# Kernel tuning notes

Hardware: AMD Instinct MI355X
Metric: run time of the kernel (lower is better)

The kernel has to match this reference:

```python
import jax, jax.numpy as jnp
import numpy as np

B, D, H = 512, 512, 512  # batch, input dim, hidden dim


def setup_inputs() -> dict:
    key = jax.random.key(0)
    ks = jax.random.split(key, 7)
    s = 1.0 / np.sqrt(D)
    return {
        "x": jax.random.normal(ks[0], (B, D), jnp.float32),
        "W1": jax.random.normal(ks[1], (D, H), jnp.float32) * s,
        "b1": jax.random.normal(ks[2], (H,), jnp.float32) * 0.01,
        "W2": jax.random.normal(ks[3], (H, H), jnp.float32) * s,
        "b2": jax.random.normal(ks[4], (H,), jnp.float32) * 0.01,
        "w3": jax.random.normal(ks[5], (H,), jnp.float32) * s,
        "b3": jax.random.normal(ks[6], (1,), jnp.float32) * 0.01,
    }


def _per_sample(xi, W1, b1, W2, b2, w3, b3):
    # Sequential layers applied to one sample; per-sample scalar loss.
    h = jax.nn.relu(xi @ W1 + b1)
    h = jax.nn.relu(h @ W2 + b2)
    return h @ w3 + b3[0]


def reference(x, W1, b1, W2, b2, w3, b3):
    # Forward pass (vectorized over the batch) -> per-sample losses [B].
    h = jax.nn.relu(x @ W1 + b1)
    h = jax.nn.relu(h @ W2 + b2)
    output = h @ w3 + b3[0]  # [B]

    # _autogram: per-sample Jacobian w.r.t. all layer parameters with a seed
    # of ones (grad = ones_like(output)); gramian accumulates J @ J.T per
    # parameter block. jax.vmap(jax.grad) == torch.vmap(vjp) with scalar seed 1.
    grad_fn = jax.grad(_per_sample, argnums=(1, 2, 3, 4, 5, 6))
    grads = jax.vmap(grad_fn, in_axes=(0, None, None, None, None, None, None))(
        x, W1, b1, W2, b2, w3, b3
    )  # pytree of per-sample grads, each leaf [B, *param_shape]

    bsz = x.shape[0]
    gramian = jnp.zeros((bsz, bsz), x.dtype)
    for g in grads:  # fixed small number of parameter tensors (matches per-layer loop)
        J = g.reshape(bsz, -1)  # [B, n_params_block]
        gramian = gramian + J @ J.T
    return output, gramian
```

## Files before the change

kernel.cpp:

```cpp
#include <hip/hip_runtime.h>


#define NN 512

typedef __attribute__((ext_vector_type(8))) short v8s;
typedef __attribute__((ext_vector_type(4))) float v4f;

static __device__ __forceinline__ unsigned short f2bf(float f) {
    union { float f; unsigned u; } v; v.f = f;
    unsigned r = v.u + 0x7FFF + ((v.u >> 16) & 1);
    return (unsigned short)(r >> 16);
}
static __device__ __forceinline__ float bf2f(unsigned short h) {
    union { unsigned u; float f; } v; v.u = ((unsigned)h) << 16;
    return v.f;
}

#define MFMA(a, b, c) __builtin_amdgcn_mfma_f32_16x16x32_bf16(a, b, c, 0, 0, 0)

__global__ __launch_bounds__(256) void prep(
    const float* __restrict__ x, const float* __restrict__ W1,
    const float* __restrict__ W2, const float* __restrict__ b3,
    unsigned short* __restrict__ xhi, unsigned short* __restrict__ xlo,
    unsigned short* __restrict__ W1th, unsigned short* __restrict__ W1tl,
    unsigned short* __restrict__ W2th, unsigned short* __restrict__ W2tl,
    unsigned short* __restrict__ W2b, float* __restrict__ out) {
    __shared__ float T[32][33];
    const int t = threadIdx.x;
    const int lr = t >> 3, lc = (t & 7) * 4;
    const int r0 = blockIdx.y * 32, c0 = blockIdx.x * 32;
    const int z = blockIdx.z;
    if (z == 2) {
        float4 v = *(const float4*)&x[(r0 + lr) * NN + c0 + lc];
        ushort4 hi, lo;
        hi.x = f2bf(v.x); lo.x = f2bf(v.x - bf2f(hi.x));
        hi.y = f2bf(v.y); lo.y = f2bf(v.y - bf2f(hi.y));
        hi.z = f2bf(v.z); lo.z = f2bf(v.z - bf2f(hi.z));
        hi.w = f2bf(v.w); lo.w = f2bf(v.w - bf2f(hi.w));
        *(ushort4*)&xhi[(r0 + lr) * NN + c0 + lc] = hi;
        *(ushort4*)&xlo[(r0 + lr) * NN + c0 + lc] = lo;
        if (blockIdx.x == 0 && t < 32) out[r0 + t] = b3[0];
        return;
    }
    const float* src = (z == 1) ? W2 : W1;
    float4 v = *(const float4*)&src[(r0 + lr) * NN + c0 + lc];
    if (z == 1) {
        ushort4 h;
        h.x = f2bf(v.x); h.y = f2bf(v.y); h.z = f2bf(v.z); h.w = f2bf(v.w);
        *(ushort4*)&W2b[(r0 + lr) * NN + c0 + lc] = h;
    }
    T[lr][lc + 0] = v.x; T[lr][lc + 1] = v.y;
    T[lr][lc + 2] = v.z; T[lr][lc + 3] = v.w;
    __syncthreads();
    unsigned short* dh = (z == 1) ? W2th : W1th;
    unsigned short* dl = (z == 1) ? W2tl : W1tl;
    float a0 = T[lc + 0][lr], a1 = T[lc + 1][lr];
    float a2 = T[lc + 2][lr], a3 = T[lc + 3][lr];
    ushort4 hi, lo;
    hi.x = f2bf(a0); lo.x = f2bf(a0 - bf2f(hi.x));
    hi.y = f2bf(a1); lo.y = f2bf(a1 - bf2f(hi.y));
    hi.z = f2bf(a2); lo.z = f2bf(a2 - bf2f(hi.z));
    hi.w = f2bf(a3); lo.w = f2bf(a3 - bf2f(hi.w));
    *(ushort4*)&dh[(c0 + lr) * NN + r0 + lc] = hi;
    *(ushort4*)&dl[(c0 + lr) * NN + r0 + lc] = lo;
}

__global__ __launch_bounds__(1024, 4) void fwd1x(
    const unsigned short* __restrict__ Ahi, const unsigned short* __restrict__ Alo,
    const unsigned short* __restrict__ Bhi, const unsigned short* __restrict__ Blo,
    const float* __restrict__ bias,
    unsigned short* __restrict__ Chi, unsigned short* __restrict__ Clo,
    float* __restrict__ SXX) {
    __shared__ float red[12][64][4];
    const int t = threadIdx.x;
    const int wave = t >> 6, lane = t & 63;
    const int q = wave & 3, s = wave >> 2;
    const int r = lane & 15, quad = lane >> 4;
    const int i0 = blockIdx.y * 32 + 16 * (q >> 1);
    const int j0 = blockIdx.x * 32 + 16 * (q & 1);
    const int ao = (i0 + r) * NN + quad * 8 + s * 128;
    const int bo = (j0 + r) * NN + quad * 8 + s * 128;
    if (blockIdx.z == 1) {
        v4f acc = {0.f, 0.f, 0.f, 0.f};
        #pragma unroll
        for (int k0 = 0; k0 < 128; k0 += 32) {
            v8s a = *(const v8s*)(Ahi + ao + k0);
            v8s b = *(const v8s*)(Ahi + bo + k0);
            acc = MFMA(a, b, acc);
        }
        if (s > 0) *(v4f*)red[(s - 1) * 4 + q][lane] = acc;
        __syncthreads();
        if (s == 0) {
            v4f a0 = acc + *(v4f*)red[q][lane] + *(v4f*)red[4 + q][lane]
                         + *(v4f*)red[8 + q][lane];
            #pragma unroll
            for (int rr = 0; rr < 4; ++rr)
                SXX[(i0 + quad * 4 + rr) * NN + j0 + r] = a0[rr];
        }
        return;
    }
    v4f hh = {0.f, 0.f, 0.f, 0.f}, lh = hh, hl = hh;
    #pragma unroll
    for (int k0 = 0; k0 < 128; k0 += 32) {
        v8s ah = *(const v8s*)(Ahi + ao + k0);
        v8s al = *(const v8s*)(Alo + ao + k0);
        v8s bh = *(const v8s*)(Bhi + bo + k0);
        v8s bl = *(const v8s*)(Blo + bo + k0);
        hh = MFMA(ah, bh, hh);
        lh = MFMA(al, bh, lh);
        hl = MFMA(ah, bl, hl);
    }
    v4f z;
    #pragma unroll
    for (int rr = 0; rr < 4; ++rr) z[rr] = (hh[rr] + lh[rr]) + hl[rr];
    if (s > 0) *(v4f*)red[(s - 1) * 4 + q][lane] = z;
    __syncthreads();
    if (s == 0) {
        v4f z0 = z + *(v4f*)red[q][lane] + *(v4f*)red[4 + q][lane]
                   + *(v4f*)red[8 + q][lane];
        const float bj = bias[j0 + r];
        #pragma unroll
        for (int rr = 0; rr < 4; ++rr) {
            const int i = i0 + quad * 4 + rr, j = j0 + r;
            float zv = z0[rr] + bj;
            float h = zv > 0.f ? zv : 0.f;
            unsigned short hi = f2bf(h);
            Chi[i * NN + j] = hi;
            Clo[i * NN + j] = f2bf(h - bf2f(hi));
        }
    }
}

__global__ __launch_bounds__(1024, 4) void fwd2(
    const unsigned short* __restrict__ Ahi, const unsigned short* __restrict__ Alo,
    const unsigned short* __restrict__ Bhi, const unsigned short* __restrict__ Blo,
    const float* __restrict__ b2, const float* __restrict__ w3,
    unsigned short* __restrict__ H2b, unsigned short* __restrict__ G2b,
    float* __restrict__ out) {
    __shared__ float red[12][64][4];
    const int t = threadIdx.x;
    const int wave = t >> 6, lane = t & 63;
    const int q = wave & 3, s = wave >> 2;
    const int r = lane & 15, quad = lane >> 4;
    const int i0 = blockIdx.y * 32 + 16 * (q >> 1);
    const int j0 = blockIdx.x * 32 + 16 * (q & 1);
    const int ao = (i0 + r) * NN + quad * 8 + s * 128;
    const int bo = (j0 + r) * NN + quad * 8 + s * 128;
    v4f hh = {0.f, 0.f, 0.f, 0.f}, lh = hh, hl = hh;
    #pragma unroll
    for (int k0 = 0; k0 < 128; k0 += 32) {
        v8s ah = *(const v8s*)(Ahi + ao + k0);
        v8s al = *(const v8s*)(Alo + ao + k0);
        v8s bh = *(const v8s*)(Bhi + bo + k0);
        v8s bl = *(const v8s*)(Blo + bo + k0);
        hh = MFMA(ah, bh, hh);
        lh = MFMA(al, bh, lh);
        hl = MFMA(ah, bl, hl);
    }
    v4f z;
    #pragma unroll
    for (int rr = 0; rr < 4; ++rr) z[rr] = (hh[rr] + lh[rr]) + hl[rr];
    if (s > 0) *(v4f*)red[(s - 1) * 4 + q][lane] = z;
    __syncthreads();
    if (s == 0) {
        v4f z0 = z + *(v4f*)red[q][lane] + *(v4f*)red[4 + q][lane]
                   + *(v4f*)red[8 + q][lane];
        const float bj = b2[j0 + r];
        const float wj = w3[j0 + r];
        const unsigned short wjb = f2bf(wj);
        #pragma unroll
        for (int rr = 0; rr < 4; ++rr) {
            const int i = i0 + quad * 4 + rr, j = j0 + r;
            float zv = z0[rr] + bj;
            float h = zv > 0.f ? zv : 0.f;
            H2b[i * NN + j] = f2bf(h);
            G2b[i * NN + j] = (zv > 0.f) ? wjb : (unsigned short)0;
            float p = h * wj;
            p += __shfl_xor(p, 1, 64);
            p += __shfl_xor(p, 2, 64);
            p += __shfl_xor(p, 4, 64);
            p += __shfl_xor(p, 8, 64);
            if (r == 0) atomicAdd(&out[i], p);
        }
    }
}

__global__ __launch_bounds__(1024, 4) void g1p(
    const unsigned short* __restrict__ G2b, const unsigned short* __restrict__ W2b,
    const unsigned short* __restrict__ H1b, const unsigned short* __restrict__ H2b,
    unsigned short* __restrict__ G1b, float* __restrict__ P) {
    __shared__ float red[12][64][3][4];
    const int t = threadIdx.x;
    const int wave = t >> 6, lane = t & 63;
    const int q = wave & 3, s = wave >> 2;
    const int r = lane & 15, quad = lane >> 4;
    const int i0 = blockIdx.y * 32 + 16 * (q >> 1);
    const int j0 = blockIdx.x * 32 + 16 * (q & 1);
    const int ao = (i0 + r) * NN + quad * 8 + s * 128;
    const int bo = (j0 + r) * NN + quad * 8 + s * 128;
    if (blockIdx.z == 1) {
        v4f a1 = {0.f, 0.f, 0.f, 0.f}, a3 = a1, a4 = a1;
        #pragma unroll
        for (int k0 = 0; k0 < 128; k0 += 32) {
            v8s ha = *(const v8s*)(H1b + ao + k0), hb = *(const v8s*)(H1b + bo + k0);
            v8s ua = *(const v8s*)(H2b + ao + k0), ub = *(const v8s*)(H2b + bo + k0);
            v8s va = *(const v8s*)(G2b + ao + k0), vb = *(const v8s*)(G2b + bo + k0);
            a1 = MFMA(ha, hb, a1);
            a3 = MFMA(ua, ub, a3);
            a4 = MFMA(va, vb, a4);
        }
        if (s > 0) {
            const int idx = (s - 1) * 4 + q;
            *(v4f*)red[idx][lane][0] = a1;
            *(v4f*)red[idx][lane][1] = a3;
            *(v4f*)red[idx][lane][2] = a4;
        }
        __syncthreads();
        if (s == 0) {
            #pragma unroll
            for (int u = 0; u < 3; ++u) {
                const int idx = u * 4 + q;
                a1 += *(v4f*)red[idx][lane][0];
                a3 += *(v4f*)red[idx][lane][1];
                a4 += *(v4f*)red[idx][lane][2];
            }
            #pragma unroll
            for (int rr = 0; rr < 4; ++rr) {
                const int i = i0 + quad * 4 + rr, j = j0 + r;
                P[i * NN + j] = a3[rr] + a4[rr] * (1.f + a1[rr]);
            }
        }
        return;
    }
    v4f acc = {0.f, 0.f, 0.f, 0.f};
    #pragma unroll
    for (int k0 = 0; k0 < 128; k0 += 32) {
        v8s a = *(const v8s*)(G2b + ao + k0);
        v8s b = *(const v8s*)(W2b + bo + k0);
        acc = MFMA(a, b, acc);
    }
    if (s > 0) *(v4f*)red[(s - 1) * 4 + q][lane][0] = acc;
    __syncthreads();
    if (s == 0) {
        v4f a0 = acc + *(v4f*)red[q][lane][0] + *(v4f*)red[4 + q][lane][0]
                     + *(v4f*)red[8 + q][lane][0];
        #pragma unroll
        for (int rr = 0; rr < 4; ++rr) {
            const int i = i0 + quad * 4 + rr;
            const int c = j0 + r;
            float v = (H1b[i * NN + c] != 0) ? a0[rr] : 0.f;
            G1b[i * NN + c] = f2bf(v);
        }
    }
}

__global__ __launch_bounds__(1024, 4) void gramf(
    const unsigned short* __restrict__ G1b, const float* __restrict__ SXX,
    const float* __restrict__ P, float* __restrict__ gram) {
    __shared__ float red[12][64][4];
    const int t = threadIdx.x;
    const int wave = t >> 6, lane = t & 63;
    const int q = wave & 3, s = wave >> 2;
    const int r = lane & 15, quad = lane >> 4;
    const int i0 = blockIdx.y * 32 + 16 * (q >> 1);
    const int j0 = blockIdx.x * 32 + 16 * (q & 1);
    const int ao = (i0 + r) * NN + quad * 8 + s * 128;
    const int bo = (j0 + r) * NN + quad * 8 + s * 128;
    v4f acc = {0.f, 0.f, 0.f, 0.f};
    #pragma unroll
    for (int k0 = 0; k0 < 128; k0 += 32) {
        v8s a = *(const v8s*)(G1b + ao + k0);
        v8s b = *(const v8s*)(G1b + bo + k0);
        acc = MFMA(a, b, acc);
    }
    if (s > 0) *(v4f*)red[(s - 1) * 4 + q][lane] = acc;
    __syncthreads();
    if (s == 0) {
        v4f a2 = acc + *(v4f*)red[q][lane] + *(v4f*)red[4 + q][lane]
                     + *(v4f*)red[8 + q][lane];
        #pragma unroll
        for (int rr = 0; rr < 4; ++rr) {
            const int i = i0 + quad * 4 + rr, j = j0 + r;
            gram[i * NN + j] = 1.f + P[i * NN + j] + a2[rr] * (1.f + SXX[i * NN + j]);
        }
    }
}

extern "C" void kernel_launch(void* const* d_in, const int* in_sizes, int n_in,
                              void* d_out, int out_size, void* d_ws, size_t ws_size,
                              hipStream_t stream) {
    const float* x  = (const float*)d_in[0];
    const float* W1 = (const float*)d_in[1];
    const float* b1 = (const float*)d_in[2];
    const float* W2 = (const float*)d_in[3];
    const float* b2 = (const float*)d_in[4];
    const float* w3 = (const float*)d_in[5];
    const float* b3 = (const float*)d_in[6];

    float* out  = (float*)d_out;
    float* gram = out + NN;

    unsigned short* p    = (unsigned short*)d_ws;
    unsigned short* xhi  = p;  p += NN * NN;
    unsigned short* xlo  = p;  p += NN * NN;
    unsigned short* W1th = p;  p += NN * NN;
    unsigned short* W1tl = p;  p += NN * NN;
    unsigned short* W2th = p;  p += NN * NN;
    unsigned short* W2tl = p;  p += NN * NN;
    unsigned short* W2b  = p;  p += NN * NN;
    unsigned short* H1b  = p;  p += NN * NN;
    unsigned short* H1lo = p;  p += NN * NN;
    unsigned short* H2b  = p;  p += NN * NN;
    unsigned short* G2b  = p;  p += NN * NN;
    unsigned short* G1b  = p;  p += NN * NN;
    float* SXX = (float*)p;  p += 2 * NN * NN;
    float* Pf  = (float*)p;  p += 2 * NN * NN;

    prep <<<dim3(16, 16, 3), dim3(256), 0, stream>>>(
        x, W1, W2, b3, xhi, xlo, W1th, W1tl, W2th, W2tl, W2b, out);
    fwd1x<<<dim3(16, 16, 2), dim3(1024), 0, stream>>>(
        xhi, xlo, W1th, W1tl, b1, H1b, H1lo, SXX);
    fwd2 <<<dim3(16, 16), dim3(1024), 0, stream>>>(
        H1b, H1lo, W2th, W2tl, b2, w3, H2b, G2b, out);
    g1p  <<<dim3(16, 16, 2), dim3(1024), 0, stream>>>(
        G2b, W2b, H1b, H2b, G1b, Pf);
    gramf<<<dim3(16, 16), dim3(1024), 0, stream>>>(
        G1b, SXX, Pf, gram);
}
```

Before: 115.8 us.

## Compute x·xᵀ Gram in prep kernel and convert x to bf16 on the fly in fwd1

Removes the xhi/xlo bf16 workspace copies of x. The x·xᵀ product (SXX) is now computed inside the prep kernel by 4-wave blocks running a full-K MFMA loop that converts fp32 x to bf16 in registers. fwd1 now loads fp32 x directly and splits it into hi/lo bf16 in registers, and drops its z=1 SXX half. This saves global writes and reads of the converted x and halves the fwd1 grid. In exchange, prep's z=2 blocks do a long serial K=512 loop with only 4 waves, and fwd1 reads twice the bytes for x and repeats the conversion.

```diff
diff --git a/kernel.cpp b/kernel.cpp
--- a/kernel.cpp
+++ b/kernel.cpp
@@ -18,30 +18,61 @@
 
 #define MFMA(a, b, c) __builtin_amdgcn_mfma_f32_16x16x32_bf16(a, b, c, 0, 0, 0)
 
+static __device__ __forceinline__ v8s load8_hi(const float* p) {
+    float4 a = *(const float4*)p;
+    float4 b = *(const float4*)(p + 4);
+    v8s h;
+    h[0] = (short)f2bf(a.x); h[1] = (short)f2bf(a.y);
+    h[2] = (short)f2bf(a.z); h[3] = (short)f2bf(a.w);
+    h[4] = (short)f2bf(b.x); h[5] = (short)f2bf(b.y);
+    h[6] = (short)f2bf(b.z); h[7] = (short)f2bf(b.w);
+    return h;
+}
+static __device__ __forceinline__ void load8_split(const float* p, v8s& h, v8s& l) {
+    float4 a = *(const float4*)p;
+    float4 b = *(const float4*)(p + 4);
+    unsigned short h0 = f2bf(a.x), h1 = f2bf(a.y), h2 = f2bf(a.z), h3 = f2bf(a.w);
+    unsigned short h4 = f2bf(b.x), h5 = f2bf(b.y), h6 = f2bf(b.z), h7 = f2bf(b.w);
+    h[0] = (short)h0; h[1] = (short)h1; h[2] = (short)h2; h[3] = (short)h3;
+    h[4] = (short)h4; h[5] = (short)h5; h[6] = (short)h6; h[7] = (short)h7;
+    l[0] = (short)f2bf(a.x - bf2f(h0)); l[1] = (short)f2bf(a.y - bf2f(h1));
+    l[2] = (short)f2bf(a.z - bf2f(h2)); l[3] = (short)f2bf(a.w - bf2f(h3));
+    l[4] = (short)f2bf(b.x - bf2f(h4)); l[5] = (short)f2bf(b.y - bf2f(h5));
+    l[6] = (short)f2bf(b.z - bf2f(h6)); l[7] = (short)f2bf(b.w - bf2f(h7));
+}
+
 __global__ __launch_bounds__(256) void prep(
     const float* __restrict__ x, const float* __restrict__ W1,
     const float* __restrict__ W2, const float* __restrict__ b3,
-    unsigned short* __restrict__ xhi, unsigned short* __restrict__ xlo,
     unsigned short* __restrict__ W1th, unsigned short* __restrict__ W1tl,
     unsigned short* __restrict__ W2th, unsigned short* __restrict__ W2tl,
-    unsigned short* __restrict__ W2b, float* __restrict__ out) {
+    unsigned short* __restrict__ W2b, float* __restrict__ SXX,
+    float* __restrict__ out) {
     __shared__ float T[32][33];
     const int t = threadIdx.x;
-    const int lr = t >> 3, lc = (t & 7) * 4;
     const int r0 = blockIdx.y * 32, c0 = blockIdx.x * 32;
     const int z = blockIdx.z;
     if (z == 2) {
-        float4 v = *(const float4*)&x[(r0 + lr) * NN + c0 + lc];
-        ushort4 hi, lo;
-        hi.x = f2bf(v.x); lo.x = f2bf(v.x - bf2f(hi.x));
-        hi.y = f2bf(v.y); lo.y = f2bf(v.y - bf2f(hi.y));
-        hi.z = f2bf(v.z); lo.z = f2bf(v.z - bf2f(hi.z));
-        hi.w = f2bf(v.w); lo.w = f2bf(v.w - bf2f(hi.w));
-        *(ushort4*)&xhi[(r0 + lr) * NN + c0 + lc] = hi;
-        *(ushort4*)&xlo[(r0 + lr) * NN + c0 + lc] = lo;
+        const int wave = t >> 6, lane = t & 63;
+        const int r = lane & 15, quad = lane >> 4;
+        const int i0 = r0 + 16 * (wave >> 1);
+        const int j0 = c0 + 16 * (wave & 1);
+        const float* ar = x + (i0 + r) * NN + quad * 8;
+        const float* br = x + (j0 + r) * NN + quad * 8;
+        v4f acc = {0.f, 0.f, 0.f, 0.f};
+        #pragma unroll
+        for (int k0 = 0; k0 < NN; k0 += 32) {
+            v8s a = load8_hi(ar + k0);
+            v8s b = load8_hi(br + k0);
+            acc = MFMA(a, b, acc);
+        }
+        #pragma unroll
+        for (int rr = 0; rr < 4; ++rr)
+            SXX[(i0 + quad * 4 + rr) * NN + j0 + r] = acc[rr];
         if (blockIdx.x == 0 && t < 32) out[r0 + t] = b3[0];
         return;
     }
+    const int lr = t >> 3, lc = (t & 7) * 4;
     const float* src = (z == 1) ? W2 : W1;
     float4 v = *(const float4*)&src[(r0 + lr) * NN + c0 + lc];
     if (z == 1) {
@@ -65,12 +96,11 @@
     *(ushort4*)&dl[(c0 + lr) * NN + r0 + lc] = lo;
 }
 
-__global__ __launch_bounds__(1024, 4) void fwd1x(
-    const unsigned short* __restrict__ Ahi, const unsigned short* __restrict__ Alo,
+__global__ __launch_bounds__(1024, 4) void fwd1(
+    const float* __restrict__ x,
     const unsigned short* __restrict__ Bhi, const unsigned short* __restrict__ Blo,
     const float* __restrict__ bias,
-    unsigned short* __restrict__ Chi, unsigned short* __restrict__ Clo,
-    float* __restrict__ SXX) {
+    unsigned short* __restrict__ Chi, unsigned short* __restrict__ Clo) {
     __shared__ float red[12][64][4];
     const int t = threadIdx.x;
     const int wave = t >> 6, lane = t & 63;
@@ -78,32 +108,13 @@
     const int r = lane & 15, quad = lane >> 4;
     const int i0 = blockIdx.y * 32 + 16 * (q >> 1);
     const int j0 = blockIdx.x * 32 + 16 * (q & 1);
-    const int ao = (i0 + r) * NN + quad * 8 + s * 128;
+    const float* ar = x + (i0 + r) * NN + quad * 8 + s * 128;
     const int bo = (j0 + r) * NN + quad * 8 + s * 128;
-    if (blockIdx.z == 1) {
-        v4f acc = {0.f, 0.f, 0.f, 0.f};
-        #pragma unroll
-        for (int k0 = 0; k0 < 128; k0 += 32) {
-            v8s a = *(const v8s*)(Ahi + ao + k0);
-            v8s b = *(const v8s*)(Ahi + bo + k0);
-            acc = MFMA(a, b, acc);
-        }
-        if (s > 0) *(v4f*)red[(s - 1) * 4 + q][lane] = acc;
-        __syncthreads();
-        if (s == 0) {
-            v4f a0 = acc + *(v4f*)red[q][lane] + *(v4f*)red[4 + q][lane]
-                         + *(v4f*)red[8 + q][lane];
-            #pragma unroll
-            for (int rr = 0; rr < 4; ++rr)
-                SXX[(i0 + quad * 4 + rr) * NN + j0 + r] = a0[rr];
-        }
-        return;
-    }
     v4f hh = {0.f, 0.f, 0.f, 0.f}, lh = hh, hl = hh;
     #pragma unroll
     for (int k0 = 0; k0 < 128; k0 += 32) {
-        v8s ah = *(const v8s*)(Ahi + ao + k0);
-        v8s al = *(const v8s*)(Alo + ao + k0);
+        v8s ah, al;
+        load8_split(ar + k0, ah, al);
         v8s bh = *(const v8s*)(Bhi + bo + k0);
         v8s bl = *(const v8s*)(Blo + bo + k0);
         hh = MFMA(ah, bh, hh);
@@ -301,8 +312,6 @@
     float* gram = out + NN;
 
     unsigned short* p    = (unsigned short*)d_ws;
-    unsigned short* xhi  = p;  p += NN * NN;
-    unsigned short* xlo  = p;  p += NN * NN;
     unsigned short* W1th = p;  p += NN * NN;
     unsigned short* W1tl = p;  p += NN * NN;
     unsigned short* W2th = p;  p += NN * NN;
@@ -317,9 +326,9 @@
     float* Pf  = (float*)p;  p += 2 * NN * NN;
 
     prep <<<dim3(16, 16, 3), dim3(256), 0, stream>>>(
-        x, W1, W2, b3, xhi, xlo, W1th, W1tl, W2th, W2tl, W2b, out);
-    fwd1x<<<dim3(16, 16, 2), dim3(1024), 0, stream>>>(
-        xhi, xlo, W1th, W1tl, b1, H1b, H1lo, SXX);
+        x, W1, W2, b3, W1th, W1tl, W2th, W2tl, W2b, SXX, out);
+    fwd1 <<<dim3(16, 16), dim3(1024), 0, stream>>>(
+        x, W1th, W1tl, b1, H1b, H1lo);
     fwd2 <<<dim3(16, 16), dim3(1024), 0, stream>>>(
         H1b, H1lo, W2th, W2tl, b2, w3, H2b, G2b, out);
     g1p  <<<dim3(16, 16, 2), dim3(1024), 0, stream>>>(
```

Measured after the change: 121.5 us. 4.9% more time.

## Drop split-K across waves; each wave computes full K with 256-thread blocks

Applied to the files above, without the earlier changes.

The four GEMM-style kernels previously used 1024-thread blocks where 4 wave groups each handled a quarter of K and reduced through shared memory with a barrier. Now each block has 4 waves, each computing its 16x16 tile over the full K=512, which removes the LDS reduction and __syncthreads. This reduces total parallelism per tile (4x fewer waves in flight) and lengthens each wave's serial MFMA chain. gramf also prefetches SXX and P before the MFMA loop to overlap those loads.

```diff
diff --git a/kernel.cpp b/kernel.cpp
--- a/kernel.cpp
+++ b/kernel.cpp
@@ -65,43 +65,35 @@
     *(ushort4*)&dl[(c0 + lr) * NN + r0 + lc] = lo;
 }
 
-__global__ __launch_bounds__(1024, 4) void fwd1x(
+__global__ __launch_bounds__(256) void fwd1x(
     const unsigned short* __restrict__ Ahi, const unsigned short* __restrict__ Alo,
     const unsigned short* __restrict__ Bhi, const unsigned short* __restrict__ Blo,
     const float* __restrict__ bias,
     unsigned short* __restrict__ Chi, unsigned short* __restrict__ Clo,
     float* __restrict__ SXX) {
-    __shared__ float red[12][64][4];
-    const int t = threadIdx.x;
-    const int wave = t >> 6, lane = t & 63;
-    const int q = wave & 3, s = wave >> 2;
-    const int r = lane & 15, quad = lane >> 4;
-    const int i0 = blockIdx.y * 32 + 16 * (q >> 1);
-    const int j0 = blockIdx.x * 32 + 16 * (q & 1);
-    const int ao = (i0 + r) * NN + quad * 8 + s * 128;
-    const int bo = (j0 + r) * NN + quad * 8 + s * 128;
+    const int t = threadIdx.x;
+    const int wave = t >> 6, lane = t & 63;
+    const int r = lane & 15, quad = lane >> 4;
+    const int i0 = blockIdx.y * 32 + 16 * (wave >> 1);
+    const int j0 = blockIdx.x * 32 + 16 * (wave & 1);
+    const int ao = (i0 + r) * NN + quad * 8;
+    const int bo = (j0 + r) * NN + quad * 8;
     if (blockIdx.z == 1) {
         v4f acc = {0.f, 0.f, 0.f, 0.f};
         #pragma unroll
-        for (int k0 = 0; k0 < 128; k0 += 32) {
+        for (int k0 = 0; k0 < NN; k0 += 32) {
             v8s a = *(const v8s*)(Ahi + ao + k0);
             v8s b = *(const v8s*)(Ahi + bo + k0);
             acc = MFMA(a, b, acc);
         }
-        if (s > 0) *(v4f*)red[(s - 1) * 4 + q][lane] = acc;
-        __syncthreads();
-        if (s == 0) {
-            v4f a0 = acc + *(v4f*)red[q][lane] + *(v4f*)red[4 + q][lane]
-                         + *(v4f*)red[8 + q][lane];
-            #pragma unroll
-            for (int rr = 0; rr < 4; ++rr)
-                SXX[(i0 + quad * 4 + rr) * NN + j0 + r] = a0[rr];
-        }
+        #pragma unroll
+        for (int rr = 0; rr < 4; ++rr)
+            SXX[(i0 + quad * 4 + rr) * NN + j0 + r] = acc[rr];
         return;
     }
     v4f hh = {0.f, 0.f, 0.f, 0.f}, lh = hh, hl = hh;
     #pragma unroll
-    for (int k0 = 0; k0 < 128; k0 += 32) {
+    for (int k0 = 0; k0 < NN; k0 += 32) {
         v8s ah = *(const v8s*)(Ahi + ao + k0);
         v8s al = *(const v8s*)(Alo + ao + k0);
         v8s bh = *(const v8s*)(Bhi + bo + k0);
@@ -110,45 +102,34 @@
         lh = MFMA(al, bh, lh);
         hl = MFMA(ah, bl, hl);
     }
-    v4f z;
-    #pragma unroll
-    for (int rr = 0; rr < 4; ++rr) z[rr] = (hh[rr] + lh[rr]) + hl[rr];
-    if (s > 0) *(v4f*)red[(s - 1) * 4 + q][lane] = z;
-    __syncthreads();
-    if (s == 0) {
-        v4f z0 = z + *(v4f*)red[q][lane] + *(v4f*)red[4 + q][lane]
-                   + *(v4f*)red[8 + q][lane];
-        const float bj = bias[j0 + r];
-        #pragma unroll
-        for (int rr = 0; rr < 4; ++rr) {
-            const int i = i0 + quad * 4 + rr, j = j0 + r;
-            float zv = z0[rr] + bj;
-            float h = zv > 0.f ? zv : 0.f;
-            unsigned short hi = f2bf(h);
-            Chi[i * NN + j] = hi;
-            Clo[i * NN + j] = f2bf(h - bf2f(hi));
-        }
-    }
-}
-
-__global__ __launch_bounds__(1024, 4) void fwd2(
+    const float bj = bias[j0 + r];
+    #pragma unroll
+    for (int rr = 0; rr < 4; ++rr) {
+        const int i = i0 + quad * 4 + rr, j = j0 + r;
+        float zv = (hh[rr] + lh[rr]) + hl[rr] + bj;
+        float h = zv > 0.f ? zv : 0.f;
+        unsigned short hi = f2bf(h);
+        Chi[i * NN + j] = hi;
+        Clo[i * NN + j] = f2bf(h - bf2f(hi));
+    }
+}
+
+__global__ __launch_bounds__(256) void fwd2(
     const unsigned short* __restrict__ Ahi, const unsigned short* __restrict__ Alo,
     const unsigned short* __restrict__ Bhi, const unsigned short* __restrict__ Blo,
     const float* __restrict__ b2, const float* __restrict__ w3,
     unsigned short* __restrict__ H2b, unsigned short* __restrict__ G2b,
     float* __restrict__ out) {
-    __shared__ float red[12][64][4];
-    const int t = threadIdx.x;
-    const int wave = t >> 6, lane = t & 63;
-    const int q = wave & 3, s = wave >> 2;
-    const int r = lane & 15, quad = lane >> 4;
-    const int i0 = blockIdx.y * 32 + 16 * (q >> 1);
-    const int j0 = blockIdx.x * 32 + 16 * (q & 1);
-    const int ao = (i0 + r) * NN + quad * 8 + s * 128;
-    const int bo = (j0 + r) * NN + quad * 8 + s * 128;
+    const int t = threadIdx.x;
+    const int wave = t >> 6, lane = t & 63;
+    const int r = lane & 15, quad = lane >> 4;
+    const int i0 = blockIdx.y * 32 + 16 * (wave >> 1);
+    const int j0 = blockIdx.x * 32 + 16 * (wave & 1);
+    const int ao = (i0 + r) * NN + quad * 8;
+    const int bo = (j0 + r) * NN + quad * 8;
     v4f hh = {0.f, 0.f, 0.f, 0.f}, lh = hh, hl = hh;
     #pragma unroll
-    for (int k0 = 0; k0 < 128; k0 += 32) {
+    for (int k0 = 0; k0 < NN; k0 += 32) {
         v8s ah = *(const v8s*)(Ahi + ao + k0);
         v8s al = *(const v8s*)(Alo + ao + k0);
         v8s bh = *(const v8s*)(Bhi + bo + k0);
@@ -157,51 +138,40 @@
         lh = MFMA(al, bh, lh);
         hl = MFMA(ah, bl, hl);
     }
-    v4f z;
-    #pragma unroll
-    for (int rr = 0; rr < 4; ++rr) z[rr] = (hh[rr] + lh[rr]) + hl[rr];
-    if (s > 0) *(v4f*)red[(s - 1) * 4 + q][lane] = z;
-    __syncthreads();
-    if (s == 0) {
-        v4f z0 = z + *(v4f*)red[q][lane] + *(v4f*)red[4 + q][lane]
-                   + *(v4f*)red[8 + q][lane];
-        const float bj = b2[j0 + r];
-        const float wj = w3[j0 + r];
-        const unsigned short wjb = f2bf(wj);
-        #pragma unroll
-        for (int rr = 0; rr < 4; ++rr) {
-            const int i = i0 + quad * 4 + rr, j = j0 + r;
-            float zv = z0[rr] + bj;
-            float h = zv > 0.f ? zv : 0.f;
-            H2b[i * NN + j] = f2bf(h);
-            G2b[i * NN + j] = (zv > 0.f) ? wjb : (unsigned short)0;
-            float p = h * wj;
-            p += __shfl_xor(p, 1, 64);
-            p += __shfl_xor(p, 2, 64);
-            p += __shfl_xor(p, 4, 64);
-            p += __shfl_xor(p, 8, 64);
-            if (r == 0) atomicAdd(&out[i], p);
-        }
-    }
-}
-
-__global__ __launch_bounds__(1024, 4) void g1p(
+    const float bj = b2[j0 + r];
+    const float wj = w3[j0 + r];
+    const unsigned short wjb = f2bf(wj);
+    #pragma unroll
+    for (int rr = 0; rr < 4; ++rr) {
+        const int i = i0 + quad * 4 + rr, j = j0 + r;
+        float zv = (hh[rr] + lh[rr]) + hl[rr] + bj;
+        float h = zv > 0.f ? zv : 0.f;
+        H2b[i * NN + j] = f2bf(h);
+        G2b[i * NN + j] = (zv > 0.f) ? wjb : (unsigned short)0;
+        float p = h * wj;
+        p += __shfl_xor(p, 1, 64);
+        p += __shfl_xor(p, 2, 64);
+        p += __shfl_xor(p, 4, 64);
+        p += __shfl_xor(p, 8, 64);
+        if (r == 0) atomicAdd(&out[i], p);
+    }
+}
+
+__global__ __launch_bounds__(256) void g1p(
     const unsigned short* __restrict__ G2b, const unsigned short* __restrict__ W2b,
     const unsigned short* __restrict__ H1b, const unsigned short* __restrict__ H2b,
     unsigned short* __restrict__ G1b, float* __restrict__ P) {
-    __shared__ float red[12][64][3][4];
-    const int t = threadIdx.x;
-    const int wave = t >> 6, lane = t & 63;
-    const int q = wave & 3, s = wave >> 2;
-    const int r = lane & 15, quad = lane >> 4;
-    const int i0 = blockIdx.y * 32 + 16 * (q >> 1);
-    const int j0 = blockIdx.x * 32 + 16 * (q & 1);
-    const int ao = (i0 + r) * NN + quad * 8 + s * 128;
-    const int bo = (j0 + r) * NN + quad * 8 + s * 128;
+    const int t = threadIdx.x;
+    const int wave = t >> 6, lane = t & 63;
+    const int r = lane & 15, quad = lane >> 4;
+    const int i0 = blockIdx.y * 32 + 16 * (wave >> 1);
+    const int j0 = blockIdx.x * 32 + 16 * (wave & 1);
+    const int ao = (i0 + r) * NN + quad * 8;
+    const int bo = (j0 + r) * NN + quad * 8;
     if (blockIdx.z == 1) {
         v4f a1 = {0.f, 0.f, 0.f, 0.f}, a3 = a1, a4 = a1;
         #pragma unroll
-        for (int k0 = 0; k0 < 128; k0 += 32) {
+        for (int k0 = 0; k0 < NN; k0 += 32) {
             v8s ha = *(const v8s*)(H1b + ao + k0), hb = *(const v8s*)(H1b + bo + k0);
             v8s ua = *(const v8s*)(H2b + ao + k0), ub = *(const v8s*)(H2b + bo + k0);
             v8s va = *(const v8s*)(G2b + ao + k0), vb = *(const v8s*)(G2b + bo + k0);
@@ -209,80 +179,57 @@
             a3 = MFMA(ua, ub, a3);
             a4 = MFMA(va, vb, a4);
         }
-        if (s > 0) {
-            const int idx = (s - 1) * 4 + q;
-            *(v4f*)red[idx][lane][0] = a1;
-            *(v4f*)red[idx][lane][1] = a3;
-            *(v4f*)red[idx][lane][2] = a4;
-        }
-        __syncthreads();
-        if (s == 0) {
-            #pragma unroll
-            for (int u = 0; u < 3; ++u) {
-                const int idx = u * 4 + q;
-                a1 += *(v4f*)red[idx][lane][0];
-                a3 += *(v4f*)red[idx][lane][1];
-                a4 += *(v4f*)red[idx][lane][2];
-            }
-            #pragma unroll
-            for (int rr = 0; rr < 4; ++rr) {
-                const int i = i0 + quad * 4 + rr, j = j0 + r;
-                P[i * NN + j] = a3[rr] + a4[rr] * (1.f + a1[rr]);
-            }
+        #pragma unroll
+        for (int rr = 0; rr < 4; ++rr) {
+            const int i = i0 + quad * 4 + rr, j = j0 + r;
+            P[i * NN + j] = a3[rr] + a4[rr] * (1.f + a1[rr]);
         }
         return;
     }
     v4f acc = {0.f, 0.f, 0.f, 0.f};
     #pragma unroll
-    for (int k0 = 0; k0 < 128; k0 += 32) {
+    for (int k0 = 0; k0 < NN; k0 += 32) {
         v8s a = *(const v8s*)(G2b + ao + k0);
         v8s b = *(const v8s*)(W2b + bo + k0);
         acc = MFMA(a, b, acc);
     }
-    if (s > 0) *(v4f*)red[(s - 1) * 4 + q][lane][0] = acc;
-    __syncthreads();
-    if (s == 0) {
-        v4f a0 = acc + *(v4f*)red[q][lane][0] + *(v4f*)red[4 + q][lane][0]
-                     + *(v4f*)red[8 + q][lane][0];
-        #pragma unroll
-        for (int rr = 0; rr < 4; ++rr) {
-            const int i = i0 + quad * 4 + rr;
-            const int c = j0 + r;
-            float v = (H1b[i * NN + c] != 0) ? a0[rr] : 0.f;
-            G1b[i * NN + c] = f2bf(v);
-        }
-    }
-}
-
-__global__ __launch_bounds__(1024, 4) void gramf(
+    #pragma unroll
+    for (int rr = 0; rr < 4; ++rr) {
+        const int i = i0 + quad * 4 + rr;
+        const int c = j0 + r;
+        float v = (H1b[i * NN + c] != 0) ? acc[rr] : 0.f;
+        G1b[i * NN + c] = f2bf(v);
+    }
+}
+
+__global__ __launch_bounds__(256) void gramf(
     const unsigned short* __restrict__ G1b, const float* __restrict__ SXX,
     const float* __restrict__ P, float* __restrict__ gram) {
-    __shared__ float red[12][64][4];
-    const int t = threadIdx.x;
-    const int wave = t >> 6, lane = t & 63;
-    const int q = wave & 3, s = wave >> 2;
-    const int r = lane & 15, quad = lane >> 4;
-    const int i0 = blockIdx.y * 32 + 16 * (q >> 1);
-    const int j0 = blockIdx.x * 32 + 16 * (q & 1);
-    const int ao = (i0 + r) * NN + quad * 8 + s * 128;
-    const int bo = (j0 + r) * NN + quad * 8 + s * 128;
+    const int t = threadIdx.x;
+    const int wave = t >> 6, lane = t & 63;
+    const int r = lane & 15, quad = lane >> 4;
+    const int i0 = blockIdx.y * 32 + 16 * (wave >> 1);
+    const int j0 = blockIdx.x * 32 + 16 * (wave & 1);
+    const int ao = (i0 + r) * NN + quad * 8;
+    const int bo = (j0 + r) * NN + quad * 8;
+    float sx[4], pp[4];
+    #pragma unroll
+    for (int rr = 0; rr < 4; ++rr) {
+        const int i = i0 + quad * 4 + rr, j = j0 + r;
+        sx[rr] = SXX[i * NN + j];
+        pp[rr] = P[i * NN + j];
+    }
     v4f acc = {0.f, 0.f, 0.f, 0.f};
     #pragma unroll
-    for (int k0 = 0; k0 < 128; k0 += 32) {
+    for (int k0 = 0; k0 < NN; k0 += 32) {
         v8s a = *(const v8s*)(G1b + ao + k0);
         v8s b = *(const v8s*)(G1b + bo + k0);
         acc = MFMA(a, b, acc);
     }
-    if (s > 0) *(v4f*)red[(s - 1) * 4 + q][lane] = acc;
-    __syncthreads();
-    if (s == 0) {
-        v4f a2 = acc + *(v4f*)red[q][lane] + *(v4f*)red[4 + q][lane]
-                     + *(v4f*)red[8 + q][lane];
-        #pragma unroll
-        for (int rr = 0; rr < 4; ++rr) {
-            const int i = i0 + quad * 4 + rr, j = j0 + r;
-            gram[i * NN + j] = 1.f + P[i * NN + j] + a2[rr] * (1.f + SXX[i * NN + j]);
-        }
+    #pragma unroll
+    for (int rr = 0; rr < 4; ++rr) {
+        const int i = i0 + quad * 4 + rr, j = j0 + r;
+        gram[i * NN + j] = 1.f + pp[rr] + acc[rr] * (1.f + sx[rr]);
     }
 }
 
@@ -316,14 +263,15 @@
     float* SXX = (float*)p;  p += 2 * NN * NN;
     float* Pf  = (float*)p;  p += 2 * NN * NN;
 
-    prep <<<dim3(16, 16, 3), dim3(256), 0, stream>>>(
+    dim3 blk(256);
+    prep <<<dim3(16, 16, 3), blk, 0, stream>>>(
         x, W1, W2, b3, xhi, xlo, W1th, W1tl, W2th, W2tl, W2b, out);
-    fwd1x<<<dim3(16, 16, 2), dim3(1024), 0, stream>>>(
+    fwd1x<<<dim3(16, 16, 2), blk, 0, stream>>>(
         xhi, xlo, W1th, W1tl, b1, H1b, H1lo, SXX);
-    fwd2 <<<dim3(16, 16), dim3(1024), 0, stream>>>(
+    fwd2 <<<dim3(16, 16), blk, 0, stream>>>(
         H1b, H1lo, W2th, W2tl, b2, w3, H2b, G2b, out);
-    g1p  <<<dim3(16, 16, 2), dim3(1024), 0, stream>>>(
+    g1p  <<<dim3(16, 16, 2), blk, 0, stream>>>(
         G2b, W2b, H1b, H2b, G1b, Pf);
-    gramf<<<dim3(16, 16), dim3(1024), 0, stream>>>(
+    gramf<<<dim3(16, 16), blk, 0, stream>>>(
         G1b, SXX, Pf, gram);
 }
```

New measurement: 114.7 us. Within noise of the previous version (-1.0%).
